# Kernel optimization log

Measured on AMD Instinct MI355X. Metric: run time of the kernel, lower is better.

Reference implementation:

```python
import jax, jax.numpy as jnp
import numpy as np

B, CL, H, W, NP = 128, 8, 16, 16, 32   # batch, primary cap length, height, width, n primary capsules
NC, CLO, ITER = 10, 16, 3              # n output capsules, output capsule length, routing iterations


def squash(t):
    # TensorMONK Activations 'squash': squash along axis 2 of a 3D tensor
    ss = jnp.sum(t * t, axis=2, keepdims=True)
    return (ss / (1.0 + ss)) * t / jnp.sqrt(ss)


def setup_inputs() -> dict:
    key = jax.random.key(0)
    k1, k2 = jax.random.split(key)
    tensor = jax.random.normal(k1, (B, CL, H, W, NP), dtype=jnp.float32)
    # nn.Parameter(torch.randn(...).normal_(0.0, 0.1)) -> N(0, 0.1)
    weight = 0.1 * jax.random.normal(k2, (CL * H * W, NP, NC * CLO), dtype=jnp.float32)
    return {"tensor": tensor, "weight": weight}


def reference(tensor, weight):
    b, cl, h, w, n_prim = tensor.shape
    # flatten spatial/length dims, squash along primary-capsule axis (dim 2, faithful to source)
    x = squash(tensor.reshape(b, -1, n_prim))                  # (B, P, N) with P = cl*h*w
    # (B,P,1,N) @ (P,N,K) broadcasted matmul -> (B,P,K)
    u = jnp.einsum('bpn,pnk->bpk', x, weight)
    u = u.reshape(b, cl, h, w, NC, CLO)                        # (B, cl, h, w, NC, CLO)
    bias = jnp.zeros((b, cl, h, w, NC), dtype=tensor.dtype)
    v = None
    for i in range(ITER):  # fixed small iteration count
        c = jax.nn.softmax(bias, axis=4)                       # softmax over output capsules
        s = jnp.einsum('bchwn,bchwnk->bnk', c, u)              # weighted sum over cl,h,w
        v = squash(s)                                          # squash along capsule length (axis 2)
        if i < ITER - 1:
            bias = bias + jnp.einsum('bchwnk,bnk->bchwn', u, v)
    return v
```

## Files before the change

kernel.cpp:

```cpp
#include <hip/hip_runtime.h>
#include <cstdint>

typedef unsigned short u16;
typedef __attribute__((ext_vector_type(8))) short bf16x8;
typedef __attribute__((ext_vector_type(4))) float f32x4;

#define B_   128
#define P_   2048
#define NC_  10
#define F_   160
#define NBLK 512
#define PPB  4
#define NTHR 512
#define WLS  162

__device__ __forceinline__ u16 f2bf(float f) {
    union { float f; unsigned u; } v; v.f = f;
    unsigned r = v.u + 0x7FFFu + ((v.u >> 16) & 1u);
    return (u16)(r >> 16);
}
__device__ __forceinline__ float bf2f(u16 h) {
    union { unsigned u; float f; } v; v.u = ((unsigned)h) << 16;
    return v.f;
}

__device__ __forceinline__ void gl_lds16(const void* g, void* l) {
    typedef __attribute__((address_space(3))) unsigned lds_uint;
    typedef __attribute__((address_space(1))) const unsigned glob_uint;
    __builtin_amdgcn_global_load_lds((glob_uint*)(uintptr_t)g,
                                     (lds_uint*)(unsigned)(uintptr_t)l, 16, 0, 0);
}

__global__ void k_prep(const float* __restrict__ t, const float* __restrict__ w,
                       u16* __restrict__ xb, u16* __restrict__ wb) {
    const int blk = blockIdx.x, tid = threadIdx.x;
    if (blk < 4096) {
        int g = blk * 256 + tid;
        int pair = g >> 2, sub = g & 3;
        int p = pair & 2047, b = pair >> 11;
        const float4* tg = (const float4*)t;
        int fi = pair * 8 + sub * 2;
        float4 va = tg[fi], vb = tg[fi + 1];
        float ss = va.x*va.x + va.y*va.y + va.z*va.z + va.w*va.w
                 + vb.x*vb.x + vb.y*vb.y + vb.z*vb.z + vb.w*vb.w;
        ss += __shfl_xor(ss, 1);
        ss += __shfl_xor(ss, 2);
        float fct = ss / ((1.f + ss) * sqrtf(ss));
        u16 h[8] __attribute__((aligned(16)));
        h[0]=f2bf(va.x*fct); h[1]=f2bf(va.y*fct); h[2]=f2bf(va.z*fct); h[3]=f2bf(va.w*fct);
        h[4]=f2bf(vb.x*fct); h[5]=f2bf(vb.y*fct); h[6]=f2bf(vb.z*fct); h[7]=f2bf(vb.w*fct);
        int off = (sub + (b >> 1)) & 3;
        *(uint4*)(xb + p * 4096 + b * 32 + off * 8) = *(const uint4*)h;
    } else {
        __shared__ u16 wl[32 * WLS];
        int p = blk - 4096;
        const float4* wp = (const float4*)(w + p * 32 * F_);
        for (int e4 = tid; e4 < 1280; e4 += 256) {
            float4 v = wp[e4];
            int k = e4 / 40, fg = e4 % 40;
            u16 h[4] __attribute__((aligned(8)));
            h[0]=f2bf(v.x); h[1]=f2bf(v.y); h[2]=f2bf(v.z); h[3]=f2bf(v.w);
            *(ushort4*)(wl + k * WLS + fg * 4) = *(const ushort4*)h;
        }
        __syncthreads();
        u16* wo = wb + p * 5120;
        for (int sid = tid; sid < 640; sid += 256) {
            int f = sid >> 2, k0 = (sid & 3) << 3, q = sid & 3;
            u16 tmp[8] __attribute__((aligned(16)));
#pragma unroll
            for (int j = 0; j < 8; ++j) tmp[j] = wl[(k0 + j) * WLS + f];
            int off = (q + (f >> 1)) & 3;
            *(uint4*)(wo + f * 32 + off * 8) = *(const uint4*)tmp;
        }
    }
}

template<int PP, int MODE>
__device__ __forceinline__ void tile_step(
    const u16* __restrict__ xt, const u16* __restrict__ wt,
    f32x4 (&s_acc)[NC_], const float4 (&vv)[NC_],
    int wv, int b, int col, int off8)
{
    if (wv < 2) __builtin_amdgcn_s_waitcnt(0x0f70 | (3 * (3 - PP)));
    else        __builtin_amdgcn_s_waitcnt(0x0f70 | (2 * (3 - PP)));
    __builtin_amdgcn_s_barrier();

    bf16x8 bfrag = *(const bf16x8*)&xt[b * 32 + off8];
    if (MODE == 0) {
#pragma unroll
        for (int n = 0; n < NC_; ++n) {
            bf16x8 afrag = *(const bf16x8*)&wt[(n * 16 + col) * 32 + off8];
            s_acc[n] = __builtin_amdgcn_mfma_f32_16x16x32_bf16(afrag, bfrag, s_acc[n], 0, 0, 0);
        }
    } else {
        float tt[NC_];
#pragma unroll
        for (int n = 0; n < NC_; ++n) {
            bf16x8 afrag = *(const bf16x8*)&wt[(n * 16 + col) * 32 + off8];
            f32x4 z = {0.f, 0.f, 0.f, 0.f};
            f32x4 acc = __builtin_amdgcn_mfma_f32_16x16x32_bf16(afrag, bfrag, z, 0, 0, 0);
            float t = acc[0]*vv[n].x + acc[1]*vv[n].y + acc[2]*vv[n].z + acc[3]*vv[n].w;
            t += __shfl_xor(t, 16);
            t += __shfl_xor(t, 32);
            tt[n] = t;
        }
        float mx = tt[0];
#pragma unroll
        for (int n = 1; n < NC_; ++n) mx = fmaxf(mx, tt[n]);
        float den = 0.f;
#pragma unroll
        for (int n = 0; n < NC_; ++n) { tt[n] = __expf(tt[n] - mx); den += tt[n]; }
        float inv = 1.f / den;
#pragma unroll
        for (int n = 0; n < NC_; ++n) {
            bf16x8 afrag = *(const bf16x8*)&wt[(n * 16 + col) * 32 + off8];
            f32x4 z = {0.f, 0.f, 0.f, 0.f};
            f32x4 acc = __builtin_amdgcn_mfma_f32_16x16x32_bf16(afrag, bfrag, z, 0, 0, 0);
            float cf = tt[n] * inv;
#pragma unroll
            for (int r = 0; r < 4; ++r) s_acc[n][r] += cf * acc[r];
        }
    }
}

template<int MODE>
__global__ __launch_bounds__(NTHR, 2) void k_pass(
        const u16* __restrict__ xb, const u16* __restrict__ wb,
        const float* __restrict__ vprev, u16* __restrict__ s_part)
{
    __shared__ __align__(16) u16 xt[PPB][4096];
    __shared__ __align__(16) u16 wt[PPB][5120];
    const int tid = threadIdx.x, blk = blockIdx.x;
    const int L = tid & 63, wv = tid >> 6;
    const int q = L >> 4, col = L & 15;
    const int b = wv * 16 + col;
    const int p0 = blk * PPB;
    const int off8 = ((q + (col >> 1)) & 3) * 8;

    float4 vv[NC_];
    if (MODE != 0) {
#pragma unroll
        for (int n = 0; n < NC_; ++n)
            vv[n] = *(const float4*)(vprev + b * F_ + n * 16 + q * 4);
    }

#pragma unroll
    for (int t = 0; t < PPB; ++t) {
        int p = p0 + t;
        gl_lds16(xb + p * 4096 + wv * 512 + L * 8, &xt[t][wv * 512]);
        gl_lds16(wb + p * 5120 + wv * 512 + L * 8, &wt[t][wv * 512]);
        if (wv < 2)
            gl_lds16(wb + p * 5120 + (8 + wv) * 512 + L * 8, &wt[t][(8 + wv) * 512]);
    }

    f32x4 s_acc[NC_];
#pragma unroll
    for (int n = 0; n < NC_; ++n) s_acc[n] = (f32x4){0.f, 0.f, 0.f, 0.f};

    tile_step<0, MODE>(xt[0], wt[0], s_acc, vv, wv, b, col, off8);
    tile_step<1, MODE>(xt[1], wt[1], s_acc, vv, wv, b, col, off8);
    tile_step<2, MODE>(xt[2], wt[2], s_acc, vv, wv, b, col, off8);
    tile_step<3, MODE>(xt[3], wt[3], s_acc, vv, wv, b, col, off8);

    __syncthreads();
    u16* ls = &wt[0][0];
    const float sc = (MODE == 0) ? 0.1f : 1.f;
#pragma unroll
    for (int n = 0; n < NC_; ++n) {
        u16 h[4] __attribute__((aligned(8)));
#pragma unroll
        for (int r = 0; r < 4; ++r) h[r] = f2bf(s_acc[n][r] * sc);
        *(ushort4*)&ls[b * F_ + n * 16 + q * 4] = *(const ushort4*)h;
    }
    __syncthreads();
    const uint4* lsv = (const uint4*)ls;
    uint4* gp = (uint4*)(s_part + blk * (B_ * F_));
#pragma unroll
    for (int i = 0; i < 5; ++i)
        gp[i * 512 + tid] = lsv[i * 512 + tid];
}

template<int ADD>
__global__ void k_red(const u16* __restrict__ s_part,
                      const float* __restrict__ vprev, float* __restrict__ vout) {
    __shared__ float r0s[256], r1s[256];
    const int tid = threadIdx.x, blk = blockIdx.x;
    const int pid = tid & 31, part = tid >> 5;
    const uint* sp = (const uint*)s_part;
    const int opair = blk * 32 + pid;
    float a0 = 0.f, a1 = 0.f;
#pragma unroll 8
    for (int g = part; g < NBLK; g += 8) {
        uint u = sp[g * 10240 + opair];
        a0 += bf2f((u16)(u & 0xffff));
        a1 += bf2f((u16)(u >> 16));
    }
    r0s[tid] = a0; r1s[tid] = a1;
    __syncthreads();
    if (tid < 32) {
        float s0 = 0.f, s1 = 0.f;
#pragma unroll
        for (int k = 0; k < 8; ++k) { s0 += r0s[k * 32 + tid]; s1 += r1s[k * 32 + tid]; }
        float sq = s0 * s0 + s1 * s1;
        sq += __shfl_xor(sq, 1);
        sq += __shfl_xor(sq, 2);
        sq += __shfl_xor(sq, 4);
        float fct = sq / ((1.f + sq) * sqrtf(sq));
        float2 o = make_float2(s0 * fct, s1 * fct);
        if (ADD) {
            float2 pv = *(const float2*)(vprev + 2 * (blk * 32 + tid));
            o.x += pv.x; o.y += pv.y;
        }
        *(float2*)(vout + 2 * (blk * 32 + tid)) = o;
    }
}

extern "C" void kernel_launch(void* const* d_in, const int* in_sizes, int n_in,
                              void* d_out, int out_size, void* d_ws, size_t ws_size,
                              hipStream_t stream) {
    const float* tensor = (const float*)d_in[0];
    const float* weight = (const float*)d_in[1];
    float* out = (float*)d_out;
    char* ws = (char*)d_ws;

    u16*   xb     = (u16*)(ws);
    u16*   wb     = (u16*)(ws + 16777216);
    u16*   s_part = (u16*)(ws + 37748736);
    float* v0     = (float*)(ws + 58720256);
    float* vs     = (float*)(ws + 58802176);

    k_prep<<<6144, 256, 0, stream>>>(tensor, weight, xb, wb);

    k_pass<0><<<NBLK, NTHR, 0, stream>>>(xb, wb, nullptr, s_part);
    k_red<0><<<320, 256, 0, stream>>>(s_part, nullptr, v0);
    k_pass<1><<<NBLK, NTHR, 0, stream>>>(xb, wb, v0, s_part);
    k_red<1><<<320, 256, 0, stream>>>(s_part, v0, vs);
    k_pass<2><<<NBLK, NTHR, 0, stream>>>(xb, wb, vs, s_part);
    k_red<0><<<320, 256, 0, stream>>>(s_part, nullptr, out);
}
```

Measured before the change: 179.0 us.

## Fuse reduction into routing pass via atomic counter and coalesce prep writes

Reduction blocks are appended to each routing-pass grid and wait on a global atomic counter incremented by producer blocks, removing three separate reduction launches. The prep kernel now squashes x in LDS tiles of 64 primary positions by 16 batches so that writes to the transposed layout are contiguous. The spin-wait relies on producer blocks making progress while consumer blocks occupy slots, which risks stalls if residency is limited.

```diff
diff --git a/kernel.cpp b/kernel.cpp
--- a/kernel.cpp
+++ b/kernel.cpp
@@ -5,14 +5,16 @@
 typedef __attribute__((ext_vector_type(8))) short bf16x8;
 typedef __attribute__((ext_vector_type(4))) float f32x4;
 
-#define B_   128
-#define P_   2048
-#define NC_  10
-#define F_   160
-#define NBLK 512
-#define PPB  4
-#define NTHR 512
-#define WLS  162
+#define B_    128
+#define P_    2048
+#define NC_   10
+#define F_    160
+#define NPROD 512
+#define NRED  80
+#define PPB   4
+#define NTHR  512
+#define WLS   162
+#define XTS   520
 
 __device__ __forceinline__ u16 f2bf(float f) {
     union { float f; unsigned u; } v; v.f = f;
@@ -32,28 +34,43 @@
 }
 
 __global__ void k_prep(const float* __restrict__ t, const float* __restrict__ w,
-                       u16* __restrict__ xb, u16* __restrict__ wb) {
+                       u16* __restrict__ xb, u16* __restrict__ wb,
+                       int* __restrict__ cnt) {
     const int blk = blockIdx.x, tid = threadIdx.x;
-    if (blk < 4096) {
-        int g = blk * 256 + tid;
-        int pair = g >> 2, sub = g & 3;
-        int p = pair & 2047, b = pair >> 11;
+    if (blk == 0 && tid < 3) cnt[tid] = 0;
+    if (blk < 256) {
+        __shared__ u16 tile[64 * XTS];
+        const int pt = blk >> 3, bt = blk & 7;
+        const int p0 = pt * 64, b0 = bt * 16;
+        const int pl = tid >> 2, sub = tid & 3;
         const float4* tg = (const float4*)t;
-        int fi = pair * 8 + sub * 2;
-        float4 va = tg[fi], vb = tg[fi + 1];
-        float ss = va.x*va.x + va.y*va.y + va.z*va.z + va.w*va.w
-                 + vb.x*vb.x + vb.y*vb.y + vb.z*vb.z + vb.w*vb.w;
-        ss += __shfl_xor(ss, 1);
-        ss += __shfl_xor(ss, 2);
-        float fct = ss / ((1.f + ss) * sqrtf(ss));
-        u16 h[8] __attribute__((aligned(16)));
-        h[0]=f2bf(va.x*fct); h[1]=f2bf(va.y*fct); h[2]=f2bf(va.z*fct); h[3]=f2bf(va.w*fct);
-        h[4]=f2bf(vb.x*fct); h[5]=f2bf(vb.y*fct); h[6]=f2bf(vb.z*fct); h[7]=f2bf(vb.w*fct);
-        int off = (sub + (b >> 1)) & 3;
-        *(uint4*)(xb + p * 4096 + b * 32 + off * 8) = *(const uint4*)h;
+#pragma unroll
+        for (int bl = 0; bl < 16; ++bl) {
+            int b = b0 + bl;
+            int fi = (b * P_ + p0 + pl) * 8 + sub * 2;
+            float4 va = tg[fi], vb = tg[fi + 1];
+            float ss = va.x*va.x + va.y*va.y + va.z*va.z + va.w*va.w
+                     + vb.x*vb.x + vb.y*vb.y + vb.z*vb.z + vb.w*vb.w;
+            ss += __shfl_xor(ss, 1);
+            ss += __shfl_xor(ss, 2);
+            float fct = ss / ((1.f + ss) * sqrtf(ss));
+            u16 h[8] __attribute__((aligned(16)));
+            h[0]=f2bf(va.x*fct); h[1]=f2bf(va.y*fct); h[2]=f2bf(va.z*fct); h[3]=f2bf(va.w*fct);
+            h[4]=f2bf(vb.x*fct); h[5]=f2bf(vb.y*fct); h[6]=f2bf(vb.z*fct); h[7]=f2bf(vb.w*fct);
+            int off = (sub + (bl >> 1)) & 3;
+            *(uint4*)&tile[pl * XTS + bl * 32 + off * 8] = *(const uint4*)h;
+        }
+        __syncthreads();
+        const int wv = tid >> 6, L = tid & 63;
+#pragma unroll
+        for (int it = 0; it < 16; ++it) {
+            int p = p0 + it * 4 + wv;
+            *(uint4*)(xb + p * 4096 + b0 * 32 + L * 8) =
+                *(const uint4*)&tile[(it * 4 + wv) * XTS + L * 8];
+        }
     } else {
         __shared__ u16 wl[32 * WLS];
-        int p = blk - 4096;
+        int p = blk - 256;
         const float4* wp = (const float4*)(w + p * 32 * F_);
         for (int e4 = tid; e4 < 1280; e4 += 256) {
             float4 v = wp[e4];
@@ -126,92 +143,103 @@
 template<int MODE>
 __global__ __launch_bounds__(NTHR, 2) void k_pass(
         const u16* __restrict__ xb, const u16* __restrict__ wb,
-        const float* __restrict__ vprev, u16* __restrict__ s_part)
+        const float* __restrict__ vprev, u16* __restrict__ s_part,
+        int* __restrict__ cnt, float* __restrict__ vout)
 {
     __shared__ __align__(16) u16 xt[PPB][4096];
     __shared__ __align__(16) u16 wt[PPB][5120];
     const int tid = threadIdx.x, blk = blockIdx.x;
-    const int L = tid & 63, wv = tid >> 6;
-    const int q = L >> 4, col = L & 15;
-    const int b = wv * 16 + col;
-    const int p0 = blk * PPB;
-    const int off8 = ((q + (col >> 1)) & 3) * 8;
-
-    float4 vv[NC_];
-    if (MODE != 0) {
-#pragma unroll
-        for (int n = 0; n < NC_; ++n)
-            vv[n] = *(const float4*)(vprev + b * F_ + n * 16 + q * 4);
-    }
-
-#pragma unroll
-    for (int t = 0; t < PPB; ++t) {
-        int p = p0 + t;
-        gl_lds16(xb + p * 4096 + wv * 512 + L * 8, &xt[t][wv * 512]);
-        gl_lds16(wb + p * 5120 + wv * 512 + L * 8, &wt[t][wv * 512]);
-        if (wv < 2)
-            gl_lds16(wb + p * 5120 + (8 + wv) * 512 + L * 8, &wt[t][(8 + wv) * 512]);
-    }
-
-    f32x4 s_acc[NC_];
-#pragma unroll
-    for (int n = 0; n < NC_; ++n) s_acc[n] = (f32x4){0.f, 0.f, 0.f, 0.f};
-
-    tile_step<0, MODE>(xt[0], wt[0], s_acc, vv, wv, b, col, off8);
-    tile_step<1, MODE>(xt[1], wt[1], s_acc, vv, wv, b, col, off8);
-    tile_step<2, MODE>(xt[2], wt[2], s_acc, vv, wv, b, col, off8);
-    tile_step<3, MODE>(xt[3], wt[3], s_acc, vv, wv, b, col, off8);
-
-    __syncthreads();
-    u16* ls = &wt[0][0];
-    const float sc = (MODE == 0) ? 0.1f : 1.f;
-#pragma unroll
-    for (int n = 0; n < NC_; ++n) {
-        u16 h[4] __attribute__((aligned(8)));
-#pragma unroll
-        for (int r = 0; r < 4; ++r) h[r] = f2bf(s_acc[n][r] * sc);
-        *(ushort4*)&ls[b * F_ + n * 16 + q * 4] = *(const ushort4*)h;
-    }
-    __syncthreads();
-    const uint4* lsv = (const uint4*)ls;
-    uint4* gp = (uint4*)(s_part + blk * (B_ * F_));
-#pragma unroll
-    for (int i = 0; i < 5; ++i)
-        gp[i * 512 + tid] = lsv[i * 512 + tid];
-}
-
-template<int ADD>
-__global__ void k_red(const u16* __restrict__ s_part,
-                      const float* __restrict__ vprev, float* __restrict__ vout) {
-    __shared__ float r0s[256], r1s[256];
-    const int tid = threadIdx.x, blk = blockIdx.x;
-    const int pid = tid & 31, part = tid >> 5;
-    const uint* sp = (const uint*)s_part;
-    const int opair = blk * 32 + pid;
-    float a0 = 0.f, a1 = 0.f;
+
+    if (blk < NPROD) {
+        const int L = tid & 63, wv = tid >> 6;
+        const int q = L >> 4, col = L & 15;
+        const int b = wv * 16 + col;
+        const int p0 = blk * PPB;
+        const int off8 = ((q + (col >> 1)) & 3) * 8;
+
+        float4 vv[NC_];
+        if (MODE != 0) {
+#pragma unroll
+            for (int n = 0; n < NC_; ++n)
+                vv[n] = *(const float4*)(vprev + b * F_ + n * 16 + q * 4);
+        }
+#pragma unroll
+        for (int t = 0; t < PPB; ++t) {
+            int p = p0 + t;
+            gl_lds16(xb + p * 4096 + wv * 512 + L * 8, &xt[t][wv * 512]);
+            gl_lds16(wb + p * 5120 + wv * 512 + L * 8, &wt[t][wv * 512]);
+            if (wv < 2)
+                gl_lds16(wb + p * 5120 + (8 + wv) * 512 + L * 8, &wt[t][(8 + wv) * 512]);
+        }
+
+        f32x4 s_acc[NC_];
+#pragma unroll
+        for (int n = 0; n < NC_; ++n) s_acc[n] = (f32x4){0.f, 0.f, 0.f, 0.f};
+
+        tile_step<0, MODE>(xt[0], wt[0], s_acc, vv, wv, b, col, off8);
+        tile_step<1, MODE>(xt[1], wt[1], s_acc, vv, wv, b, col, off8);
+        tile_step<2, MODE>(xt[2], wt[2], s_acc, vv, wv, b, col, off8);
+        tile_step<3, MODE>(xt[3], wt[3], s_acc, vv, wv, b, col, off8);
+
+        __syncthreads();
+        u16* ls = &wt[0][0];
+        const float sc = (MODE == 0) ? 0.1f : 1.f;
+#pragma unroll
+        for (int n = 0; n < NC_; ++n) {
+            u16 h[4] __attribute__((aligned(8)));
+#pragma unroll
+            for (int r = 0; r < 4; ++r) h[r] = f2bf(s_acc[n][r] * sc);
+            *(ushort4*)&ls[b * F_ + n * 16 + q * 4] = *(const ushort4*)h;
+        }
+        __syncthreads();
+        const uint4* lsv = (const uint4*)ls;
+        uint4* gp = (uint4*)(s_part + blk * (B_ * F_));
+#pragma unroll
+        for (int i = 0; i < 5; ++i)
+            gp[i * 512 + tid] = lsv[i * 512 + tid];
+
+        __syncthreads();
+        if (tid == 0) {
+            __threadfence();
+            atomicAdd(cnt, 1);
+        }
+    } else {
+        const int rblk = blk - NPROD;
+        if (tid == 0) {
+            while (__hip_atomic_load(cnt, __ATOMIC_RELAXED,
+                                     __HIP_MEMORY_SCOPE_AGENT) < NPROD)
+                __builtin_amdgcn_s_sleep(16);
+            __threadfence();
+        }
+        __syncthreads();
+        const int pid = tid & 127, part = tid >> 7;
+        const int o = rblk * 128 + pid;
+        const uint* sp = (const uint*)s_part;
+        float a0 = 0.f, a1 = 0.f;
 #pragma unroll 8
-    for (int g = part; g < NBLK; g += 8) {
-        uint u = sp[g * 10240 + opair];
-        a0 += bf2f((u16)(u & 0xffff));
-        a1 += bf2f((u16)(u >> 16));
-    }
-    r0s[tid] = a0; r1s[tid] = a1;
-    __syncthreads();
-    if (tid < 32) {
-        float s0 = 0.f, s1 = 0.f;
-#pragma unroll
-        for (int k = 0; k < 8; ++k) { s0 += r0s[k * 32 + tid]; s1 += r1s[k * 32 + tid]; }
-        float sq = s0 * s0 + s1 * s1;
-        sq += __shfl_xor(sq, 1);
-        sq += __shfl_xor(sq, 2);
-        sq += __shfl_xor(sq, 4);
-        float fct = sq / ((1.f + sq) * sqrtf(sq));
-        float2 o = make_float2(s0 * fct, s1 * fct);
-        if (ADD) {
-            float2 pv = *(const float2*)(vprev + 2 * (blk * 32 + tid));
-            o.x += pv.x; o.y += pv.y;
-        }
-        *(float2*)(vout + 2 * (blk * 32 + tid)) = o;
+        for (int g = part; g < NPROD; g += 4) {
+            uint u = sp[g * 10240 + o];
+            a0 += bf2f((u16)(u & 0xffff));
+            a1 += bf2f((u16)(u >> 16));
+        }
+        float* rs = (float*)&xt[0][0];
+        rs[tid] = a0; rs[512 + tid] = a1;
+        __syncthreads();
+        if (tid < 128) {
+            float s0 = rs[tid] + rs[tid + 128] + rs[tid + 256] + rs[tid + 384];
+            float s1 = rs[512 + tid] + rs[640 + tid] + rs[768 + tid] + rs[896 + tid];
+            float sq = s0 * s0 + s1 * s1;
+            sq += __shfl_xor(sq, 1);
+            sq += __shfl_xor(sq, 2);
+            sq += __shfl_xor(sq, 4);
+            float fct = sq / ((1.f + sq) * sqrtf(sq));
+            float2 res = make_float2(s0 * fct, s1 * fct);
+            if (MODE == 1) {
+                float2 pv = *(const float2*)(vprev + 2 * o);
+                res.x += pv.x; res.y += pv.y;
+            }
+            *(float2*)(vout + 2 * o) = res;
+        }
     }
 }
 
@@ -228,13 +256,11 @@
     u16*   s_part = (u16*)(ws + 37748736);
     float* v0     = (float*)(ws + 58720256);
     float* vs     = (float*)(ws + 58802176);
-
-    k_prep<<<6144, 256, 0, stream>>>(tensor, weight, xb, wb);
-
-    k_pass<0><<<NBLK, NTHR, 0, stream>>>(xb, wb, nullptr, s_part);
-    k_red<0><<<320, 256, 0, stream>>>(s_part, nullptr, v0);
-    k_pass<1><<<NBLK, NTHR, 0, stream>>>(xb, wb, v0, s_part);
-    k_red<1><<<320, 256, 0, stream>>>(s_part, v0, vs);
-    k_pass<2><<<NBLK, NTHR, 0, stream>>>(xb, wb, vs, s_part);
-    k_red<0><<<320, 256, 0, stream>>>(s_part, nullptr, out);
-}
+    int*   cnt    = (int*)(ws + 58884096);
+
+    k_prep<<<2304, 256, 0, stream>>>(tensor, weight, xb, wb, cnt);
+
+    k_pass<0><<<NPROD + NRED, NTHR, 0, stream>>>(xb, wb, nullptr, s_part, cnt + 0, v0);
+    k_pass<1><<<NPROD + NRED, NTHR, 0, stream>>>(xb, wb, v0,      s_part, cnt + 1, vs);
+    k_pass<2><<<NPROD + NRED, NTHR, 0, stream>>>(xb, wb, vs,      s_part, cnt + 2, out);
+}
```

Result: slower. 279.0 us (+55.9%).
